# Performance work log

Measured on AMD Instinct MI355X. Metric: run time of the kernel, lower is better.

The kernel has to match this reference:

```python
import jax, jax.numpy as jnp
import numpy as np

N = 25000      # n_nodes
K = 16         # k_sparse (out-degree per node)
E = N * K      # n_edges
D = 12         # depth
U = 48         # units
FEATS = 2
EF = 1
EPS = 1e-5     # BatchNorm eps


def _lin(h, W, b):
    return h @ W.T + b


def _bn(h, g, b):
    # training-mode BatchNorm over dim 0 (biased variance, like torch)
    m = h.mean(0)
    v = jnp.mean((h - m) ** 2, axis=0)
    return (h - m) * jax.lax.rsqrt(v + EPS) * g + b


def setup_inputs():
    key = jax.random.key(0)
    ks = iter(jax.random.split(key, 64))

    def nrm(shape, fan):
        return jax.random.normal(next(ks), shape, dtype=jnp.float32) * float(1.0 / np.sqrt(fan))

    inp = {}
    inp['x'] = jax.random.uniform(next(ks), (N, FEATS), dtype=jnp.float32)
    inp['edge_attr'] = jax.random.uniform(next(ks), (E, EF), dtype=jnp.float32)
    src = jnp.repeat(jnp.arange(N, dtype=jnp.int32), K)            # each node has K out-edges
    dst = jax.random.randint(next(ks), (E,), 0, N, dtype=jnp.int32)
    inp['edge_index'] = jnp.stack([src, dst])                       # [2, E]
    inp['v_lin0_W'] = nrm((U, FEATS), FEATS); inp['v_lin0_b'] = nrm((U,), FEATS)
    for nm in ['vW1', 'vW2', 'vW3', 'vW4']:
        inp[nm] = nrm((D, U, U), U)
    for nm in ['vb1', 'vb2', 'vb3', 'vb4']:
        inp[nm] = nrm((D, U), U)
    inp['vbn_g'] = jnp.ones((D, U), jnp.float32); inp['vbn_b'] = jnp.zeros((D, U), jnp.float32)
    inp['e_lin0_W'] = nrm((U, EF), EF); inp['e_lin0_b'] = nrm((U,), EF)
    inp['eW'] = nrm((D, U, U), U); inp['eb'] = nrm((D, U), U)
    inp['ebn_g'] = jnp.ones((D, U), jnp.float32); inp['ebn_b'] = jnp.zeros((D, U), jnp.float32)
    inp['pW0'] = nrm((U, U), U); inp['pb0'] = nrm((U,), U)
    inp['pW1'] = nrm((U, U), U); inp['pb1'] = nrm((U,), U)
    inp['pW2'] = nrm((1, U), U); inp['pb2'] = nrm((1,), U)
    inp['zW0'] = nrm((U, U), U); inp['zb0'] = nrm((U,), U)
    inp['zW1'] = nrm((1, U), U); inp['zb1'] = nrm((1,), U)
    inp['k_sparse'] = K
    return inp


def _forward(edge_index, k_sparse, x, edge_attr, v_lin0_W, v_lin0_b, vW1, vb1, vW2, vb2, vW3, vb3, vW4, vb4, vbn_g, vbn_b, e_lin0_W, e_lin0_b, eW, eb, ebn_g, ebn_b, pW0, pb0, pW1, pb1, pW2, pb2, zW0, zb0, zW1, zb1):
    n = x.shape[0]
    src, dst = edge_index[0], edge_index[1]
    deg = jnp.maximum(jax.ops.segment_sum(jnp.ones((src.shape[0],), x.dtype), src, num_segments=n), 1.0)
    h = jax.nn.silu(_lin(x, v_lin0_W, v_lin0_b))          # [N, U]
    w = jax.nn.silu(_lin(edge_attr, e_lin0_W, e_lin0_b))  # [E, U]

    def layer(carry, p):
        h, w = carry
        W1, b1, W2, b2, W3, b3, W4, b4, gv, bv, We, be, ge, bee = p
        h1 = _lin(h, W1, b1); h2 = _lin(h, W2, b2)
        h3 = _lin(h, W3, b3); h4 = _lin(h, W4, b4)
        msg = jax.nn.sigmoid(w) * h2[dst]                                 # [E, U] gather + gate
        agg = jax.ops.segment_sum(msg, src, num_segments=n) / deg[:, None]  # scatter-mean to source node
        h_new = h + jax.nn.silu(_bn(h1 + agg, gv, bv))
        w_new = w + jax.nn.silu(_bn(_lin(w, We, be) + h3[src] + h4[dst], ge, bee))
        return (h_new, w_new), None

    (_, w), _ = jax.lax.scan(layer, (h, w), (vW1, vb1, vW2, vb2, vW3, vb3, vW4, vb4, vbn_g, vbn_b, eW, eb, ebn_g, ebn_b))

    # ParNet heuristic head: MLP then group-softmax over k_sparse edges per node
    p = jax.nn.silu(_lin(w, pW0, pb0))
    p = jax.nn.silu(_lin(p, pW1, pb1))
    p = _lin(p, pW2, pb2).reshape(-1, k_sparse)
    heu = jax.nn.softmax(p, axis=1).reshape(-1)                            # [E]
    # Z_net logZ head (mean over edges)
    logZ = jnp.mean(jax.nn.relu(_lin(w, zW0, zb0)) @ zW1.T + zb1, axis=0)  # [1]
    return heu, logZ


def reference(x, edge_attr, edge_index, v_lin0_W, v_lin0_b, vW1, vb1, vW2, vb2, vW3, vb3, vW4, vb4, vbn_g, vbn_b, e_lin0_W, e_lin0_b, eW, eb, ebn_g, ebn_b, pW0, pb0, pW1, pb1, pW2, pb2, zW0, zb0, zW1, zb1, k_sparse):
    return _forward(edge_index, k_sparse, x, edge_attr, v_lin0_W, v_lin0_b, vW1, vb1, vW2, vb2, vW3, vb3, vW4, vb4, vbn_g, vbn_b, e_lin0_W, e_lin0_b, eW, eb, ebn_g, ebn_b, pW0, pb0, pW1, pb1, pW2, pb2, zW0, zb0, zW1, zb1)
```

## Files before the change

kernel.cpp:

```cpp
#include <hip/hip_runtime.h>
#include <hip/hip_bf16.h>

#define NN 25000
#define KK 16
#define EE 400000
#define DD 12
#define UU 48
#define EPSBN 1e-5f
#define RP 88

using bf16 = __hip_bfloat16;
typedef short bf16x8 __attribute__((ext_vector_type(8)));
typedef float f32x4 __attribute__((ext_vector_type(4)));

__device__ __forceinline__ float b2f(bf16 v){ return __bfloat162float(v); }
__device__ __forceinline__ float sigm(float x){ return 1.f/(1.f+__expf(-x)); }
__device__ __forceinline__ float siluf(float x){ return x/(1.f+__expf(-x)); }
__device__ __forceinline__ short f2bs(float f){ bf16 h=__float2bfloat16(f); return *(short*)&h; }
__device__ __forceinline__ float bs2f(short s){ bf16 h; *(short*)&h = s; return __bfloat162float(h); }

__device__ __forceinline__ float ldx(const void* p, size_t i, bool isb){
  return isb ? b2f(((const bf16*)p)[i]) : ((const float*)p)[i];
}
__device__ __forceinline__ void stout(void* p, size_t i, float v, bool isb){
  if (isb) ((bf16*)p)[i] = __float2bfloat16(v);
  else     ((float*)p)[i] = v;
}
__device__ __forceinline__ bool dflag(const void* vbng){
  return *((const unsigned*)vbng) == 0x3F803F80u;
}
#define LDSFENCE() asm volatile("s_waitcnt lgkmcnt(0)" ::: "memory")

__global__ void k_init_nodes(const void* __restrict__ x, const void* __restrict__ W0,
                             const void* __restrict__ b0, float* __restrict__ h,
                             float* __restrict__ stats, float* __restrict__ zpart,
                             const void* __restrict__ fl){
  const bool isb = dflag(fl);
  int gid = blockIdx.x*256 + threadIdx.x;
  if (gid < DD*12288) stats[gid] = 0.f;
  if (gid < 64) zpart[gid] = 0.f;
  if (gid < NN*UU){
    int n = gid/UU, c = gid%UU;
    float acc = ldx(b0,c,isb) + ldx(W0,c*2,isb)*ldx(x,n*2,isb) + ldx(W0,c*2+1,isb)*ldx(x,n*2+1,isb);
    h[gid] = siluf(acc);
  }
}

__global__ void k_init_edges(const void* __restrict__ ea, const void* __restrict__ W0,
                             const void* __restrict__ b0, float* __restrict__ w,
                             const void* __restrict__ fl){
  const bool isb = dflag(fl);
  int gid = blockIdx.x*256 + threadIdx.x;
  if (gid < EE*UU){
    int e = gid/UU, c = gid%UU;
    float acc = ldx(b0,c,isb) + ldx(W0,c,isb)*ldx(ea,e,isb);
    w[gid] = siluf(acc);
  }
}

__global__ __launch_bounds__(256) void k_node(
    float* __restrict__ h, float* __restrict__ h1,
    short* __restrict__ h2b, short* __restrict__ h3b, short* __restrict__ h4b,
    const void* __restrict__ W1, const void* __restrict__ W2,
    const void* __restrict__ W3, const void* __restrict__ W4,
    const void* __restrict__ b1, const void* __restrict__ b2,
    const void* __restrict__ b3, const void* __restrict__ b4,
    const void* __restrict__ gv, const void* __restrict__ bv,
    const float* __restrict__ stats, int ctl, const void* __restrict__ fl)
{
  const bool isb = dflag(fl);
  const int d = ctl>>1, apply = ctl&1;
  const size_t WOFF = (size_t)d*UU*UU, BOFF = (size_t)d*UU;
  __shared__ alignas(16) short BT[4][48*RP];
  __shared__ alignas(16) short AT[4][16*RP];
  __shared__ float bL[4][UU];
  __shared__ float scV[96];
  __shared__ float sred[96];
  int tid = threadIdx.x, lane = tid&63, wid = tid>>6;
  const void* Ws[4] = {W1,W2,W3,W4};
  const void* bs[4] = {b1,b2,b3,b4};
  for (int i=tid;i<4*2304;i+=256){ int m=i/2304, j=i%2304; int r=j/48,k=j%48;
    BT[m][r*RP+k]=f2bs(ldx(Ws[m],WOFF+j,isb)); }
  for (int i=tid;i<4*768;i+=256){ int m=i/768, j=i%768; int r=j/16,k=48+(j%16); BT[m][r*RP+k]=0; }
  for (int i=tid;i<4*256;i+=256){ int wv=i/256, j=i%256; int r=j/16,k=48+(j%16); AT[wv][r*RP+k]=0; }
  if (tid<192) bL[tid/48][tid%48] = ldx(bs[tid/48],BOFF+(tid%48),isb);
  if (apply && tid<96){
    const float* sp = stats + (size_t)(d-1)*12288;
    float s=0.f;
    for (int k2=0;k2<64;k2++) s += sp[k2*96+tid];
    sred[tid]=s;
  }
  __syncthreads();
  if (apply && tid<48){
    float mean = sred[tid]/(float)NN;
    float var = sred[48+tid]/(float)NN - mean*mean; if (var<0.f) var=0.f;
    float sc = ldx(gv,(size_t)(d-1)*48+tid,isb) * rsqrtf(var+EPSBN);
    scV[tid]=sc; scV[48+tid]=ldx(bv,(size_t)(d-1)*48+tid,isb) - mean*sc;
  }
  __syncthreads();

  int quad = lane>>4, lrow = lane&15;
  short* A = AT[wid];
  int gw = blockIdx.x*4+wid, gws = gridDim.x*4;
  const int NT = (NN+15)/16;
  for (int t=gw; t<NT; t+=gws){
    int nb = t*16;
    #pragma unroll
    for (int j=0;j<3;j++){
      int f = lane+64*j; int r=f/12, c4=f%12; int n=nb+r;
      short4 s4; s4.x=0;s4.y=0;s4.z=0;s4.w=0;
      if (n<NN){
        size_t gi = (size_t)n*48 + c4*4;
        float4 hv = *(const float4*)&h[gi];
        if (apply){
          float4 yv = *(const float4*)&h1[gi];
          int c0=c4*4;
          hv.x += siluf(scV[c0+0]*yv.x + scV[48+c0+0]);
          hv.y += siluf(scV[c0+1]*yv.y + scV[48+c0+1]);
          hv.z += siluf(scV[c0+2]*yv.z + scV[48+c0+2]);
          hv.w += siluf(scV[c0+3]*yv.w + scV[48+c0+3]);
          *(float4*)&h[gi] = hv;
        }
        s4.x=f2bs(hv.x); s4.y=f2bs(hv.y); s4.z=f2bs(hv.z); s4.w=f2bs(hv.w);
      }
      *(short4*)&A[r*RP + c4*4] = s4;
    }
    LDSFENCE();
    bf16x8 a0 = *(const bf16x8*)&A[lrow*RP + quad*8];
    bf16x8 a1 = *(const bf16x8*)&A[lrow*RP + 32 + quad*8];
    #pragma unroll
    for (int m=0;m<4;m++){
      f32x4 ac0={0,0,0,0}, ac1={0,0,0,0}, ac2={0,0,0,0};
      bf16x8 bfr;
      bfr = *(const bf16x8*)&BT[m][(0+lrow)*RP + quad*8];      ac0=__builtin_amdgcn_mfma_f32_16x16x32_bf16(a0,bfr,ac0,0,0,0);
      bfr = *(const bf16x8*)&BT[m][(0+lrow)*RP + 32 + quad*8]; ac0=__builtin_amdgcn_mfma_f32_16x16x32_bf16(a1,bfr,ac0,0,0,0);
      bfr = *(const bf16x8*)&BT[m][(16+lrow)*RP + quad*8];     ac1=__builtin_amdgcn_mfma_f32_16x16x32_bf16(a0,bfr,ac1,0,0,0);
      bfr = *(const bf16x8*)&BT[m][(16+lrow)*RP + 32 + quad*8];ac1=__builtin_amdgcn_mfma_f32_16x16x32_bf16(a1,bfr,ac1,0,0,0);
      bfr = *(const bf16x8*)&BT[m][(32+lrow)*RP + quad*8];     ac2=__builtin_amdgcn_mfma_f32_16x16x32_bf16(a0,bfr,ac2,0,0,0);
      bfr = *(const bf16x8*)&BT[m][(32+lrow)*RP + 32 + quad*8];ac2=__builtin_amdgcn_mfma_f32_16x16x32_bf16(a1,bfr,ac2,0,0,0);
      #pragma unroll
      for (int nt=0;nt<3;nt++){
        int c = nt*16+lrow;
        f32x4 ac = (nt==0)?ac0:((nt==1)?ac1:ac2);
        float bv2 = bL[m][c];
        #pragma unroll
        for (int r=0;r<4;r++){
          int n = nb + quad*4 + r;
          if (n<NN){
            float v = ac[r] + bv2;
            if (m==0) h1[(size_t)n*48+c] = v;
            else if (m==1) h2b[(size_t)n*48+c] = f2bs(v);
            else if (m==2) h3b[(size_t)n*48+c] = f2bs(v);
            else           h4b[(size_t)n*48+c] = f2bs(v);
          }
        }
      }
    }
  }
}

__global__ __launch_bounds__(256) void k_edge(
    float* __restrict__ w, short* __restrict__ tmp,
    float* __restrict__ h1, const short* __restrict__ h2b,
    const short* __restrict__ h3b, const short* __restrict__ h4b,
    const int* __restrict__ dst,
    const void* __restrict__ We, const void* __restrict__ eb,
    const void* __restrict__ ge, const void* __restrict__ be,
    float* __restrict__ stats, int ctl, const void* __restrict__ fl)
{
  const bool isb = dflag(fl);
  const int d = ctl>>1, apply = ctl&1;
  const size_t WOFF = (size_t)d*UU*UU, BOFF = (size_t)d*UU;
  __shared__ alignas(16) short BT[48*RP];
  __shared__ alignas(16) short AT[4][16*RP];
  __shared__ float ebL[UU];
  __shared__ float scE[96];
  __shared__ float sred[96];
  __shared__ float sACC[4][192];
  int tid = threadIdx.x, lane = tid&63, wid = tid>>6;
  for (int i=tid;i<2304;i+=256){ int r=i/48,k=i%48; BT[r*RP+k]=f2bs(ldx(We,WOFF+i,isb)); }
  for (int i=tid;i<768;i+=256){ int r=i/16,k=48+(i%16); BT[r*RP+k]=0; }
  for (int i=tid;i<4*256;i+=256){ int wv=i/256, j=i%256; int r=j/16,k=48+(j%16); AT[wv][r*RP+k]=0; }
  if (tid<48) ebL[tid]=ldx(eb,BOFF+tid,isb);
  for (int i=tid;i<768;i+=256) ((float*)sACC)[i]=0.f;
  if (apply && tid<96){
    const float* sp = stats + (size_t)(d-1)*12288 + 6144;
    float s=0.f;
    for (int k2=0;k2<64;k2++) s += sp[k2*96+tid];
    sred[tid]=s;
  }
  __syncthreads();
  if (apply && tid<48){
    float mean = sred[tid]/(float)EE;
    float var = sred[48+tid]/(float)EE - mean*mean; if (var<0.f) var=0.f;
    float sc = ldx(ge,(size_t)(d-1)*48+tid,isb) * rsqrtf(var+EPSBN);
    scE[tid]=sc; scE[48+tid]=ldx(be,(size_t)(d-1)*48+tid,isb) - mean*sc;
  }
  __syncthreads();

  int quad = lane>>4, lrow = lane&15;
  short* A = AT[wid];
  float* myStats = stats + (size_t)d*12288;
  float accY[3]={0,0,0}, accY2[3]={0,0,0}, accT[3]={0,0,0}, accT2[3]={0,0,0};
  int gw = blockIdx.x*4+wid, gws = gridDim.x*4;
  for (int n=gw; n<NN; n+=gws){
    size_t basef = (size_t)n*768;
    int de[4];
    #pragma unroll
    for (int r=0;r<4;r++) de[r] = dst[n*16 + quad*4 + r];
    #pragma unroll
    for (int j=0;j<3;j++){
      int f = lane+64*j; int r=f/12, c4=f%12;
      size_t gi = basef + r*48 + c4*4;
      float4 wv = *(const float4*)&w[gi];
      if (apply){
        short4 t4 = *(const short4*)&tmp[gi];
        int c0=c4*4;
        wv.x += siluf(scE[c0+0]*bs2f(t4.x) + scE[48+c0+0]);
        wv.y += siluf(scE[c0+1]*bs2f(t4.y) + scE[48+c0+1]);
        wv.z += siluf(scE[c0+2]*bs2f(t4.z) + scE[48+c0+2]);
        wv.w += siluf(scE[c0+3]*bs2f(t4.w) + scE[48+c0+3]);
        *(float4*)&w[gi] = wv;
      }
      short4 s4; s4.x=f2bs(wv.x); s4.y=f2bs(wv.y); s4.z=f2bs(wv.z); s4.w=f2bs(wv.w);
      *(short4*)&A[r*RP + c4*4] = s4;
    }
    LDSFENCE();
    bf16x8 a0 = *(const bf16x8*)&A[lrow*RP + quad*8];
    bf16x8 a1 = *(const bf16x8*)&A[lrow*RP + 32 + quad*8];
    f32x4 ac0={0,0,0,0}, ac1={0,0,0,0}, ac2={0,0,0,0};
    bf16x8 bfr;
    bfr = *(const bf16x8*)&BT[(0+lrow)*RP + quad*8];      ac0=__builtin_amdgcn_mfma_f32_16x16x32_bf16(a0,bfr,ac0,0,0,0);
    bfr = *(const bf16x8*)&BT[(0+lrow)*RP + 32 + quad*8]; ac0=__builtin_amdgcn_mfma_f32_16x16x32_bf16(a1,bfr,ac0,0,0,0);
    bfr = *(const bf16x8*)&BT[(16+lrow)*RP + quad*8];     ac1=__builtin_amdgcn_mfma_f32_16x16x32_bf16(a0,bfr,ac1,0,0,0);
    bfr = *(const bf16x8*)&BT[(16+lrow)*RP + 32 + quad*8];ac1=__builtin_amdgcn_mfma_f32_16x16x32_bf16(a1,bfr,ac1,0,0,0);
    bfr = *(const bf16x8*)&BT[(32+lrow)*RP + quad*8];     ac2=__builtin_amdgcn_mfma_f32_16x16x32_bf16(a0,bfr,ac2,0,0,0);
    bfr = *(const bf16x8*)&BT[(32+lrow)*RP + 32 + quad*8];ac2=__builtin_amdgcn_mfma_f32_16x16x32_bf16(a1,bfr,ac2,0,0,0);
    #pragma unroll
    for (int nt=0;nt<3;nt++){
      int c = nt*16+lrow;
      f32x4 ac = (nt==0)?ac0:((nt==1)?ac1:ac2);
      float bv = ebL[c];
      float h3v = bs2f(h3b[(size_t)n*48+c]);
      float pT=0.f, pT2=0.f, pM=0.f;
      #pragma unroll
      for (int r=0;r<4;r++){
        int e = quad*4+r;
        float t = ac[r] + bv + h3v + bs2f(h4b[(size_t)de[r]*48+c]);
        pT += t; pT2 += t*t;
        float wv = bs2f(A[e*RP+c]);
        A[e*RP+c] = f2bs(t);
        pM += bs2f(h2b[(size_t)de[r]*48+c]) * sigm(wv);
      }
      pT  += __shfl_xor(pT,16);  pT  += __shfl_xor(pT,32);
      pT2 += __shfl_xor(pT2,16); pT2 += __shfl_xor(pT2,32);
      pM  += __shfl_xor(pM,16);  pM  += __shfl_xor(pM,32);
      accT[nt] += pT; accT2[nt] += pT2;
      if (lane<16){
        float yv = h1[(size_t)n*48+c] + pM*(1.f/16.f);
        h1[(size_t)n*48+c] = yv;
        accY[nt] += yv; accY2[nt] += yv*yv;
      }
    }
    LDSFENCE();
    #pragma unroll
    for (int j=0;j<2;j++){
      int idx = lane + 64*j;
      if (idx < 96){
        int r = idx/6, c8 = idx%6;
        *(bf16x8*)&tmp[basef + r*48 + c8*8] = *(const bf16x8*)&A[r*RP + c8*8];
      }
    }
  }
  if (lane<16){
    #pragma unroll
    for (int nt=0;nt<3;nt++){
      int c = nt*16+lane;
      sACC[wid][c]      = accY[nt];
      sACC[wid][48+c]   = accY2[nt];
      sACC[wid][96+c]   = accT[nt];
      sACC[wid][144+c]  = accT2[nt];
    }
  }
  __syncthreads();
  if (tid<192){
    float s = sACC[0][tid]+sACC[1][tid]+sACC[2][tid]+sACC[3][tid];
    int bk = (blockIdx.x&63)*96;
    if (tid<96) atomicAdd(&myStats[bk+tid], s);
    else        atomicAdd(&myStats[6144+bk+(tid-96)], s);
  }
}

__global__ __launch_bounds__(256) void k_head1(
    const float* __restrict__ w, short* __restrict__ tmp,
    const void* __restrict__ pW0, const void* __restrict__ pb0,
    const void* __restrict__ zW0, const void* __restrict__ zb0,
    const void* __restrict__ zW1,
    const void* __restrict__ ge, const void* __restrict__ be,
    const float* __restrict__ stats, float* __restrict__ zpart,
    const void* __restrict__ fl)
{
  const bool isb = dflag(fl);
  __shared__ alignas(16) short BT0[48*RP];
  __shared__ alignas(16) short BT1[48*RP];
  __shared__ alignas(16) short AT[4][16*RP];
  __shared__ float pb0L[UU], zb0L[UU], zW1L[UU];
  __shared__ float scE[96];
  __shared__ float sred[96];
  __shared__ float zS[4];
  int tid = threadIdx.x, lane = tid&63, wid = tid>>6;
  for (int i=tid;i<2304;i+=256){ int r=i/48,k=i%48;
    BT0[r*RP+k]=f2bs(ldx(pW0,i,isb)); BT1[r*RP+k]=f2bs(ldx(zW0,i,isb)); }
  for (int i=tid;i<768;i+=256){ int r=i/16,k=48+(i%16); BT0[r*RP+k]=0; BT1[r*RP+k]=0; }
  for (int i=tid;i<4*256;i+=256){ int wv=i/256, j=i%256; int r=j/16,k=48+(j%16); AT[wv][r*RP+k]=0; }
  if (tid<48){ pb0L[tid]=ldx(pb0,tid,isb); zb0L[tid]=ldx(zb0,tid,isb); zW1L[tid]=ldx(zW1,tid,isb); }
  if (tid<96){
    const float* sp = stats + (size_t)(DD-1)*12288 + 6144;
    float s=0.f;
    for (int k2=0;k2<64;k2++) s += sp[k2*96+tid];
    sred[tid]=s;
  }
  __syncthreads();
  if (tid<48){
    float mean = sred[tid]/(float)EE;
    float var = sred[48+tid]/(float)EE - mean*mean; if (var<0.f) var=0.f;
    float sc = ldx(ge,(size_t)(DD-1)*48+tid,isb) * rsqrtf(var+EPSBN);
    scE[tid]=sc; scE[48+tid]=ldx(be,(size_t)(DD-1)*48+tid,isb) - mean*sc;
  }
  __syncthreads();

  int quad = lane>>4, lrow = lane&15;
  short* A = AT[wid];
  float zacc = 0.f;
  int gw = blockIdx.x*4+wid, gws = gridDim.x*4;
  for (int n=gw; n<NN; n+=gws){
    size_t basef = (size_t)n*768;
    #pragma unroll
    for (int j=0;j<3;j++){
      int f = lane+64*j; int r=f/12, c4=f%12;
      size_t gi = basef + r*48 + c4*4;
      float4 wv = *(const float4*)&w[gi];
      short4 t4 = *(const short4*)&tmp[gi];
      int c0=c4*4;
      wv.x += siluf(scE[c0+0]*bs2f(t4.x) + scE[48+c0+0]);
      wv.y += siluf(scE[c0+1]*bs2f(t4.y) + scE[48+c0+1]);
      wv.z += siluf(scE[c0+2]*bs2f(t4.z) + scE[48+c0+2]);
      wv.w += siluf(scE[c0+3]*bs2f(t4.w) + scE[48+c0+3]);
      short4 s4; s4.x=f2bs(wv.x); s4.y=f2bs(wv.y); s4.z=f2bs(wv.z); s4.w=f2bs(wv.w);
      *(short4*)&A[r*RP + c4*4] = s4;
    }
    LDSFENCE();
    bf16x8 a0 = *(const bf16x8*)&A[lrow*RP + quad*8];
    bf16x8 a1 = *(const bf16x8*)&A[lrow*RP + 32 + quad*8];
    f32x4 p0={0,0,0,0}, p1={0,0,0,0}, p2={0,0,0,0};
    f32x4 z0={0,0,0,0}, z1={0,0,0,0}, z2={0,0,0,0};
    bf16x8 bfr;
    bfr=*(const bf16x8*)&BT0[(0+lrow)*RP+quad*8];       p0=__builtin_amdgcn_mfma_f32_16x16x32_bf16(a0,bfr,p0,0,0,0);
    bfr=*(const bf16x8*)&BT0[(0+lrow)*RP+32+quad*8];    p0=__builtin_amdgcn_mfma_f32_16x16x32_bf16(a1,bfr,p0,0,0,0);
    bfr=*(const bf16x8*)&BT0[(16+lrow)*RP+quad*8];      p1=__builtin_amdgcn_mfma_f32_16x16x32_bf16(a0,bfr,p1,0,0,0);
    bfr=*(const bf16x8*)&BT0[(16+lrow)*RP+32+quad*8];   p1=__builtin_amdgcn_mfma_f32_16x16x32_bf16(a1,bfr,p1,0,0,0);
    bfr=*(const bf16x8*)&BT0[(32+lrow)*RP+quad*8];      p2=__builtin_amdgcn_mfma_f32_16x16x32_bf16(a0,bfr,p2,0,0,0);
    bfr=*(const bf16x8*)&BT0[(32+lrow)*RP+32+quad*8];   p2=__builtin_amdgcn_mfma_f32_16x16x32_bf16(a1,bfr,p2,0,0,0);
    bfr=*(const bf16x8*)&BT1[(0+lrow)*RP+quad*8];       z0=__builtin_amdgcn_mfma_f32_16x16x32_bf16(a0,bfr,z0,0,0,0);
    bfr=*(const bf16x8*)&BT1[(0+lrow)*RP+32+quad*8];    z0=__builtin_amdgcn_mfma_f32_16x16x32_bf16(a1,bfr,z0,0,0,0);
    bfr=*(const bf16x8*)&BT1[(16+lrow)*RP+quad*8];      z1=__builtin_amdgcn_mfma_f32_16x16x32_bf16(a0,bfr,z1,0,0,0);
    bfr=*(const bf16x8*)&BT1[(16+lrow)*RP+32+quad*8];   z1=__builtin_amdgcn_mfma_f32_16x16x32_bf16(a1,bfr,z1,0,0,0);
    bfr=*(const bf16x8*)&BT1[(32+lrow)*RP+quad*8];      z2=__builtin_amdgcn_mfma_f32_16x16x32_bf16(a0,bfr,z2,0,0,0);
    bfr=*(const bf16x8*)&BT1[(32+lrow)*RP+32+quad*8];   z2=__builtin_amdgcn_mfma_f32_16x16x32_bf16(a1,bfr,z2,0,0,0);
    #pragma unroll
    for (int nt=0;nt<3;nt++){
      int c = nt*16+lrow;
      f32x4 pp = (nt==0)?p0:((nt==1)?p1:p2);
      f32x4 zz = (nt==0)?z0:((nt==1)?z1:z2);
      float pb = pb0L[c], zb = zb0L[c], zw = zW1L[c];
      #pragma unroll
      for (int r=0;r<4;r++){
        int e = quad*4+r;
        A[e*RP+c] = f2bs(siluf(pp[r] + pb));
        float zr = zz[r] + zb;
        zacc += zw * (zr > 0.f ? zr : 0.f);
      }
    }
    LDSFENCE();
    #pragma unroll
    for (int j=0;j<2;j++){
      int idx = lane + 64*j;
      if (idx < 96){
        int r = idx/6, c8 = idx%6;
        *(bf16x8*)&tmp[basef + r*48 + c8*8] = *(const bf16x8*)&A[r*RP + c8*8];
      }
    }
  }
  zacc += __shfl_xor(zacc,1); zacc += __shfl_xor(zacc,2); zacc += __shfl_xor(zacc,4);
  zacc += __shfl_xor(zacc,8); zacc += __shfl_xor(zacc,16); zacc += __shfl_xor(zacc,32);
  if (lane==0) zS[wid]=zacc;
  __syncthreads();
  if (tid==0) atomicAdd(&zpart[blockIdx.x&63], zS[0]+zS[1]+zS[2]+zS[3]);
}

__global__ __launch_bounds__(256) void k_head2(
    const short* __restrict__ tmp,
    const void* __restrict__ pW1, const void* __restrict__ pb1,
    const void* __restrict__ pW2,
    void* __restrict__ out, const void* __restrict__ fl)
{
  const bool isb = dflag(fl);
  __shared__ alignas(16) short BT[48*RP];
  __shared__ alignas(16) short AT[4][16*RP];
  __shared__ float pb1L[UU], pW2L[UU];
  int tid = threadIdx.x, lane = tid&63, wid = tid>>6;
  for (int i=tid;i<2304;i+=256){ int r=i/48,k=i%48; BT[r*RP+k]=f2bs(ldx(pW1,i,isb)); }
  for (int i=tid;i<768;i+=256){ int r=i/16,k=48+(i%16); BT[r*RP+k]=0; }
  for (int i=tid;i<4*256;i+=256){ int wv=i/256, j=i%256; int r=j/16,k=48+(j%16); AT[wv][r*RP+k]=0; }
  if (tid<48){ pb1L[tid]=ldx(pb1,tid,isb); pW2L[tid]=ldx(pW2,tid,isb); }
  __syncthreads();

  int quad = lane>>4, lrow = lane&15;
  short* A = AT[wid];
  int gw = blockIdx.x*4+wid, gws = gridDim.x*4;
  for (int n=gw; n<NN; n+=gws){
    size_t basef = (size_t)n*768;
    #pragma unroll
    for (int j=0;j<2;j++){
      int idx = lane + 64*j;
      if (idx < 96){
        int r = idx/6, c8 = idx%6;
        *(bf16x8*)&A[r*RP + c8*8] = *(const bf16x8*)&tmp[basef + r*48 + c8*8];
      }
    }
    LDSFENCE();
    bf16x8 a0 = *(const bf16x8*)&A[lrow*RP + quad*8];
    bf16x8 a1 = *(const bf16x8*)&A[lrow*RP + 32 + quad*8];
    f32x4 q0={0,0,0,0}, q1={0,0,0,0}, q2={0,0,0,0};
    bf16x8 bfr;
    bfr=*(const bf16x8*)&BT[(0+lrow)*RP+quad*8];       q0=__builtin_amdgcn_mfma_f32_16x16x32_bf16(a0,bfr,q0,0,0,0);
    bfr=*(const bf16x8*)&BT[(0+lrow)*RP+32+quad*8];    q0=__builtin_amdgcn_mfma_f32_16x16x32_bf16(a1,bfr,q0,0,0,0);
    bfr=*(const bf16x8*)&BT[(16+lrow)*RP+quad*8];      q1=__builtin_amdgcn_mfma_f32_16x16x32_bf16(a0,bfr,q1,0,0,0);
    bfr=*(const bf16x8*)&BT[(16+lrow)*RP+32+quad*8];   q1=__builtin_amdgcn_mfma_f32_16x16x32_bf16(a1,bfr,q1,0,0,0);
    bfr=*(const bf16x8*)&BT[(32+lrow)*RP+quad*8];      q2=__builtin_amdgcn_mfma_f32_16x16x32_bf16(a0,bfr,q2,0,0,0);
    bfr=*(const bf16x8*)&BT[(32+lrow)*RP+32+quad*8];   q2=__builtin_amdgcn_mfma_f32_16x16x32_bf16(a1,bfr,q2,0,0,0);
    float pp[4] = {0.f,0.f,0.f,0.f};
    #pragma unroll
    for (int nt=0;nt<3;nt++){
      int c = nt*16+lrow;
      f32x4 qq = (nt==0)?q0:((nt==1)?q1:q2);
      float pb = pb1L[c], pw = pW2L[c];
      #pragma unroll
      for (int r=0;r<4;r++) pp[r] += pw * siluf(qq[r] + pb);
    }
    #pragma unroll
    for (int r=0;r<4;r++){
      pp[r] += __shfl_xor(pp[r],1); pp[r] += __shfl_xor(pp[r],2);
      pp[r] += __shfl_xor(pp[r],4); pp[r] += __shfl_xor(pp[r],8);
    }
    float mx = fmaxf(fmaxf(pp[0],pp[1]), fmaxf(pp[2],pp[3]));
    mx = fmaxf(mx, __shfl_xor(mx,16)); mx = fmaxf(mx, __shfl_xor(mx,32));
    float ex[4]; float se = 0.f;
    #pragma unroll
    for (int r=0;r<4;r++){ ex[r] = __expf(pp[r]-mx); se += ex[r]; }
    se += __shfl_xor(se,16); se += __shfl_xor(se,32);
    float inv = 1.f/se;
    if (lrow==0){
      #pragma unroll
      for (int r=0;r<4;r++) stout(out, (size_t)n*16 + quad*4 + r, ex[r]*inv, isb);
    }
  }
}

__global__ void k_final(const float* __restrict__ zpart, const void* __restrict__ zb1,
                        void* __restrict__ out, const void* __restrict__ fl){
  const bool isb = dflag(fl);
  int tid=threadIdx.x;
  float s = (tid<64) ? zpart[tid] : 0.f;
  s += __shfl_xor(s,1); s += __shfl_xor(s,2); s += __shfl_xor(s,4);
  s += __shfl_xor(s,8); s += __shfl_xor(s,16); s += __shfl_xor(s,32);
  if (tid==0) stout(out, EE, s/(float)EE + ldx(zb1,0,isb), isb);
}

extern "C" void kernel_launch(void* const* d_in, const int* in_sizes, int n_in,
                              void* d_out, int out_size, void* d_ws, size_t ws_size,
                              hipStream_t stream){
  (void)in_sizes; (void)n_in; (void)out_size; (void)ws_size;
  const void* x=d_in[0]; const void* ea=d_in[1];
  const int* ei=(const int*)d_in[2];
  const void* vW0=d_in[3]; const void* vb0=d_in[4];
  const void* vW1=d_in[5]; const void* vW2=d_in[6]; const void* vW3=d_in[7]; const void* vW4=d_in[8];
  const void* vb1=d_in[9]; const void* vb2=d_in[10]; const void* vb3=d_in[11]; const void* vb4=d_in[12];
  const void* vbng=d_in[13]; const void* vbnb=d_in[14];
  const void* eW0=d_in[15]; const void* eb0=d_in[16];
  const void* eW=d_in[17]; const void* ebv=d_in[18];
  const void* ebng=d_in[19]; const void* ebnb=d_in[20];
  const void* pW0=d_in[21]; const void* pb0=d_in[22];
  const void* pW1=d_in[23]; const void* pb1=d_in[24];
  const void* pW2=d_in[25]; const void* pb2=d_in[26]; (void)pb2;
  const void* zW0=d_in[27]; const void* zb0=d_in[28];
  const void* zW1=d_in[29]; const void* zb1=d_in[30];
  const int* dst = ei + EE;
  const void* fl = vbng;

  float* h   = (float*)d_ws;
  float* h1  = h  + (size_t)NN*UU;
  short* h2b = (short*)(h1 + (size_t)NN*UU);
  short* h3b = h2b + (size_t)NN*UU;
  short* h4b = h3b + (size_t)NN*UU;
  float* w   = (float*)(h4b + (size_t)NN*UU);
  short* tmp = (short*)(w + (size_t)EE*UU);
  float* stats = (float*)(tmp + (size_t)EE*UU);
  float* zpart = stats + DD*12288;

  k_init_nodes<<<(NN*UU+255)/256,256,0,stream>>>(x,vW0,vb0,h,stats,zpart,fl);
  k_init_edges<<<(EE*UU+255)/256,256,0,stream>>>(ea,eW0,eb0,w,fl);
  for (int d=0; d<DD; d++){
    int ctl = (d<<1) | (d>0 ? 1 : 0);
    k_node<<<512,256,0,stream>>>(h,h1,h2b,h3b,h4b,
        vW1,vW2,vW3,vW4,vb1,vb2,vb3,vb4,vbng,vbnb,stats,ctl,fl);
    k_edge<<<1536,256,0,stream>>>(w,tmp,h1,h2b,h3b,h4b,dst,eW,ebv,ebng,ebnb,stats,ctl,fl);
  }
  k_head1<<<1536,256,0,stream>>>(w,tmp,pW0,pb0,zW0,zb0,zW1,ebng,ebnb,stats,zpart,fl);
  k_head2<<<1536,256,0,stream>>>(tmp,pW1,pb1,pW2,d_out,fl);
  k_final<<<1,64,0,stream>>>(zpart,zb1,d_out,fl);
}
```

Measured before the change: 1.417 ms.

## Prefetch next node's edge data, use nontemporal streams and fp16 intermediates

```diff
diff --git a/kernel.cpp b/kernel.cpp
--- a/kernel.cpp
+++ b/kernel.cpp
@@ -1,5 +1,6 @@
 #include <hip/hip_runtime.h>
 #include <hip/hip_bf16.h>
+#include <hip/hip_fp16.h>
 
 #define NN 25000
 #define KK 16
@@ -12,12 +13,16 @@
 using bf16 = __hip_bfloat16;
 typedef short bf16x8 __attribute__((ext_vector_type(8)));
 typedef float f32x4 __attribute__((ext_vector_type(4)));
+typedef float fx4 __attribute__((ext_vector_type(4)));
+typedef short sx4 __attribute__((ext_vector_type(4)));
 
 __device__ __forceinline__ float b2f(bf16 v){ return __bfloat162float(v); }
 __device__ __forceinline__ float sigm(float x){ return 1.f/(1.f+__expf(-x)); }
 __device__ __forceinline__ float siluf(float x){ return x/(1.f+__expf(-x)); }
 __device__ __forceinline__ short f2bs(float f){ bf16 h=__float2bfloat16(f); return *(short*)&h; }
 __device__ __forceinline__ float bs2f(short s){ bf16 h; *(short*)&h = s; return __bfloat162float(h); }
+__device__ __forceinline__ short f2hs(float f){ __half h=__float2half(f); return *(short*)&h; }
+__device__ __forceinline__ float hs2f(short s){ __half h; *(short*)&h = s; return __half2float(h); }
 
 __device__ __forceinline__ float ldx(const void* p, size_t i, bool isb){
   return isb ? b2f(((const bf16*)p)[i]) : ((const float*)p)[i];
@@ -29,6 +34,11 @@
 __device__ __forceinline__ bool dflag(const void* vbng){
   return *((const unsigned*)vbng) == 0x3F803F80u;
 }
+__device__ __forceinline__ fx4 ntlf4(const float* p){ return __builtin_nontemporal_load((const fx4*)p); }
+__device__ __forceinline__ void ntsf4(float* p, fx4 v){ __builtin_nontemporal_store(v,(fx4*)p); }
+__device__ __forceinline__ sx4 ntls4(const short* p){ return __builtin_nontemporal_load((const sx4*)p); }
+__device__ __forceinline__ bf16x8 ntls8(const short* p){ return __builtin_nontemporal_load((const bf16x8*)p); }
+__device__ __forceinline__ void ntss8(short* p, bf16x8 v){ __builtin_nontemporal_store(v,(bf16x8*)p); }
 #define LDSFENCE() asm volatile("s_waitcnt lgkmcnt(0)" ::: "memory")
 
 __global__ void k_init_nodes(const void* __restrict__ x, const void* __restrict__ W0,
@@ -149,9 +159,9 @@
           if (n<NN){
             float v = ac[r] + bv2;
             if (m==0) h1[(size_t)n*48+c] = v;
-            else if (m==1) h2b[(size_t)n*48+c] = f2bs(v);
-            else if (m==2) h3b[(size_t)n*48+c] = f2bs(v);
-            else           h4b[(size_t)n*48+c] = f2bs(v);
+            else if (m==1) h2b[(size_t)n*48+c] = f2hs(v);
+            else if (m==2) h3b[(size_t)n*48+c] = f2hs(v);
+            else           h4b[(size_t)n*48+c] = f2hs(v);
           }
         }
       }
@@ -159,7 +169,7 @@
   }
 }
 
-__global__ __launch_bounds__(256) void k_edge(
+__global__ __launch_bounds__(256,4) void k_edge(
     float* __restrict__ w, short* __restrict__ tmp,
     float* __restrict__ h1, const short* __restrict__ h2b,
     const short* __restrict__ h3b, const short* __restrict__ h4b,
@@ -203,28 +213,75 @@
   float* myStats = stats + (size_t)d*12288;
   float accY[3]={0,0,0}, accY2[3]={0,0,0}, accT[3]={0,0,0}, accT2[3]={0,0,0};
   int gw = blockIdx.x*4+wid, gws = gridDim.x*4;
+
+  int jr[3], jc[3];
+  #pragma unroll
+  for (int j=0;j<3;j++){ int f=lane+64*j; jr[j]=f/12; jc[j]=f%12; }
+
+  fx4 nW[3]; sx4 nT[3]; int4 nDe={0,0,0,0}; float nH3[3]={0,0,0};
+  if (gw < NN){
+    size_t b0=(size_t)gw*768;
+    #pragma unroll
+    for (int j=0;j<3;j++){
+      nW[j]=ntlf4(&w[b0+jr[j]*48+jc[j]*4]);
+      if (apply) nT[j]=ntls4(&tmp[b0+jr[j]*48+jc[j]*4]);
+    }
+    nDe = *(const int4*)&dst[gw*16+quad*4];
+    #pragma unroll
+    for (int nt=0;nt<3;nt++) nH3[nt]=hs2f(h3b[(size_t)gw*48+nt*16+lrow]);
+  }
+
   for (int n=gw; n<NN; n+=gws){
     size_t basef = (size_t)n*768;
-    int de[4];
-    #pragma unroll
-    for (int r=0;r<4;r++) de[r] = dst[n*16 + quad*4 + r];
+    fx4 cW[3]={nW[0],nW[1],nW[2]};
+    sx4 cT[3]={nT[0],nT[1],nT[2]};
+    int dei[4]={nDe.x,nDe.y,nDe.z,nDe.w};
+    float h3v[3]={nH3[0],nH3[1],nH3[2]};
+
     #pragma unroll
     for (int j=0;j<3;j++){
-      int f = lane+64*j; int r=f/12, c4=f%12;
-      size_t gi = basef + r*48 + c4*4;
-      float4 wv = *(const float4*)&w[gi];
+      fx4 wv = cW[j];
       if (apply){
-        short4 t4 = *(const short4*)&tmp[gi];
-        int c0=c4*4;
-        wv.x += siluf(scE[c0+0]*bs2f(t4.x) + scE[48+c0+0]);
-        wv.y += siluf(scE[c0+1]*bs2f(t4.y) + scE[48+c0+1]);
-        wv.z += siluf(scE[c0+2]*bs2f(t4.z) + scE[48+c0+2]);
-        wv.w += siluf(scE[c0+3]*bs2f(t4.w) + scE[48+c0+3]);
-        *(float4*)&w[gi] = wv;
-      }
-      short4 s4; s4.x=f2bs(wv.x); s4.y=f2bs(wv.y); s4.z=f2bs(wv.z); s4.w=f2bs(wv.w);
-      *(short4*)&A[r*RP + c4*4] = s4;
-    }
+        int c0=jc[j]*4;
+        wv[0] += siluf(scE[c0+0]*hs2f(cT[j][0]) + scE[48+c0+0]);
+        wv[1] += siluf(scE[c0+1]*hs2f(cT[j][1]) + scE[48+c0+1]);
+        wv[2] += siluf(scE[c0+2]*hs2f(cT[j][2]) + scE[48+c0+2]);
+        wv[3] += siluf(scE[c0+3]*hs2f(cT[j][3]) + scE[48+c0+3]);
+        ntsf4(&w[basef+jr[j]*48+jc[j]*4], wv);
+      }
+      short4 s4; s4.x=f2bs(wv[0]); s4.y=f2bs(wv[1]); s4.z=f2bs(wv[2]); s4.w=f2bs(wv[3]);
+      *(short4*)&A[jr[j]*RP + jc[j]*4] = s4;
+    }
+
+    float g4v[3][4], g2v[3][4];
+    #pragma unroll
+    for (int nt=0;nt<3;nt++){
+      int c = nt*16+lrow;
+      #pragma unroll
+      for (int r=0;r<4;r++){
+        g4v[nt][r] = hs2f(h4b[(size_t)dei[r]*48+c]);
+        g2v[nt][r] = hs2f(h2b[(size_t)dei[r]*48+c]);
+      }
+    }
+    float h1v[3]={0,0,0};
+    if (lane<16){
+      #pragma unroll
+      for (int nt=0;nt<3;nt++) h1v[nt]=h1[(size_t)n*48+nt*16+lane];
+    }
+
+    int n2 = n+gws;
+    if (n2 < NN){
+      size_t b2=(size_t)n2*768;
+      #pragma unroll
+      for (int j=0;j<3;j++){
+        nW[j]=ntlf4(&w[b2+jr[j]*48+jc[j]*4]);
+        if (apply) nT[j]=ntls4(&tmp[b2+jr[j]*48+jc[j]*4]);
+      }
+      nDe = *(const int4*)&dst[n2*16+quad*4];
+      #pragma unroll
+      for (int nt=0;nt<3;nt++) nH3[nt]=hs2f(h3b[(size_t)n2*48+nt*16+lrow]);
+    }
+
     LDSFENCE();
     bf16x8 a0 = *(const bf16x8*)&A[lrow*RP + quad*8];
     bf16x8 a1 = *(const bf16x8*)&A[lrow*RP + 32 + quad*8];
@@ -236,28 +293,28 @@
     bfr = *(const bf16x8*)&BT[(16+lrow)*RP + 32 + quad*8];ac1=__builtin_amdgcn_mfma_f32_16x16x32_bf16(a1,bfr,ac1,0,0,0);
     bfr = *(const bf16x8*)&BT[(32+lrow)*RP + quad*8];     ac2=__builtin_amdgcn_mfma_f32_16x16x32_bf16(a0,bfr,ac2,0,0,0);
     bfr = *(const bf16x8*)&BT[(32+lrow)*RP + 32 + quad*8];ac2=__builtin_amdgcn_mfma_f32_16x16x32_bf16(a1,bfr,ac2,0,0,0);
+
     #pragma unroll
     for (int nt=0;nt<3;nt++){
       int c = nt*16+lrow;
       f32x4 ac = (nt==0)?ac0:((nt==1)?ac1:ac2);
       float bv = ebL[c];
-      float h3v = bs2f(h3b[(size_t)n*48+c]);
       float pT=0.f, pT2=0.f, pM=0.f;
       #pragma unroll
       for (int r=0;r<4;r++){
         int e = quad*4+r;
-        float t = ac[r] + bv + h3v + bs2f(h4b[(size_t)de[r]*48+c]);
+        float t = ac[r] + bv + h3v[nt] + g4v[nt][r];
         pT += t; pT2 += t*t;
-        float wv = bs2f(A[e*RP+c]);
-        A[e*RP+c] = f2bs(t);
-        pM += bs2f(h2b[(size_t)de[r]*48+c]) * sigm(wv);
+        float gate = bs2f(A[e*RP+c]);
+        A[e*RP+c] = f2hs(t);
+        pM += g2v[nt][r] * sigm(gate);
       }
       pT  += __shfl_xor(pT,16);  pT  += __shfl_xor(pT,32);
       pT2 += __shfl_xor(pT2,16); pT2 += __shfl_xor(pT2,32);
       pM  += __shfl_xor(pM,16);  pM  += __shfl_xor(pM,32);
       accT[nt] += pT; accT2[nt] += pT2;
       if (lane<16){
-        float yv = h1[(size_t)n*48+c] + pM*(1.f/16.f);
+        float yv = h1v[nt] + pM*(1.f/16.f);
         h1[(size_t)n*48+c] = yv;
         accY[nt] += yv; accY2[nt] += yv*yv;
       }
@@ -268,7 +325,7 @@
       int idx = lane + 64*j;
       if (idx < 96){
         int r = idx/6, c8 = idx%6;
-        *(bf16x8*)&tmp[basef + r*48 + c8*8] = *(const bf16x8*)&A[r*RP + c8*8];
+        ntss8(&tmp[basef + r*48 + c8*8], *(const bf16x8*)&A[r*RP + c8*8]);
       }
     }
   }
@@ -339,14 +396,14 @@
     for (int j=0;j<3;j++){
       int f = lane+64*j; int r=f/12, c4=f%12;
       size_t gi = basef + r*48 + c4*4;
-      float4 wv = *(const float4*)&w[gi];
-      short4 t4 = *(const short4*)&tmp[gi];
+      fx4 wv = ntlf4(&w[gi]);
+      sx4 t4 = ntls4(&tmp[gi]);
       int c0=c4*4;
-      wv.x += siluf(scE[c0+0]*bs2f(t4.x) + scE[48+c0+0]);
-      wv.y += siluf(scE[c0+1]*bs2f(t4.y) + scE[48+c0+1]);
-      wv.z += siluf(scE[c0+2]*bs2f(t4.z) + scE[48+c0+2]);
-      wv.w += siluf(scE[c0+3]*bs2f(t4.w) + scE[48+c0+3]);
-      short4 s4; s4.x=f2bs(wv.x); s4.y=f2bs(wv.y); s4.z=f2bs(wv.z); s4.w=f2bs(wv.w);
+      wv[0] += siluf(scE[c0+0]*hs2f(t4[0]) + scE[48+c0+0]);
+      wv[1] += siluf(scE[c0+1]*hs2f(t4[1]) + scE[48+c0+1]);
+      wv[2] += siluf(scE[c0+2]*hs2f(t4[2]) + scE[48+c0+2]);
+      wv[3] += siluf(scE[c0+3]*hs2f(t4[3]) + scE[48+c0+3]);
+      short4 s4; s4.x=f2bs(wv[0]); s4.y=f2bs(wv[1]); s4.z=f2bs(wv[2]); s4.w=f2bs(wv[3]);
       *(short4*)&A[r*RP + c4*4] = s4;
     }
     LDSFENCE();
@@ -387,7 +444,7 @@
       int idx = lane + 64*j;
       if (idx < 96){
         int r = idx/6, c8 = idx%6;
-        *(bf16x8*)&tmp[basef + r*48 + c8*8] = *(const bf16x8*)&A[r*RP + c8*8];
+        ntss8(&tmp[basef + r*48 + c8*8], *(const bf16x8*)&A[r*RP + c8*8]);
       }
     }
   }
@@ -425,7 +482,7 @@
       int idx = lane + 64*j;
       if (idx < 96){
         int r = idx/6, c8 = idx%6;
-        *(bf16x8*)&A[r*RP + c8*8] = *(const bf16x8*)&tmp[basef + r*48 + c8*8];
+        *(bf16x8*)&A[r*RP + c8*8] = ntls8(&tmp[basef + r*48 + c8*8]);
       }
     }
     LDSFENCE();
@@ -514,9 +571,9 @@
     int ctl = (d<<1) | (d>0 ? 1 : 0);
     k_node<<<512,256,0,stream>>>(h,h1,h2b,h3b,h4b,
         vW1,vW2,vW3,vW4,vb1,vb2,vb3,vb4,vbng,vbnb,stats,ctl,fl);
-    k_edge<<<1536,256,0,stream>>>(w,tmp,h1,h2b,h3b,h4b,dst,eW,ebv,ebng,ebnb,stats,ctl,fl);
-  }
-  k_head1<<<1536,256,0,stream>>>(w,tmp,pW0,pb0,zW0,zb0,zW1,ebng,ebnb,stats,zpart,fl);
-  k_head2<<<1536,256,0,stream>>>(tmp,pW1,pb1,pW2,d_out,fl);
+    k_edge<<<1024,256,0,stream>>>(w,tmp,h1,h2b,h3b,h4b,dst,eW,ebv,ebng,ebnb,stats,ctl,fl);
+  }
+  k_head1<<<1024,256,0,stream>>>(w,tmp,pW0,pb0,zW0,zb0,zW1,ebng,ebnb,stats,zpart,fl);
+  k_head2<<<1024,256,0,stream>>>(tmp,pW1,pb1,pW2,d_out,fl);
   k_final<<<1,64,0,stream>>>(zpart,zb1,d_out,fl);
 }
```

Result: no change. 1.412 ms (-0.3%).
